# Kernel optimization log

Measured on AMD Instinct MI355X. Metric: run time of the kernel, lower is better.

## Reference

```python
import jax, jax.numpy as jnp
import numpy as np

B, S, H, NH = 2, 2048, 1024, 16
HD = H // NH
SCALE = float(H) ** 0.5  # note: source scales by sqrt(hidden_dim), not sqrt(head_dim)
EPS = 1e-5


def setup_inputs() -> dict:
    key = jax.random.key(0)
    ks = jax.random.split(key, 16)
    s = 0.02
    return {
        "q": jax.random.normal(ks[0], (B, S, H), jnp.float32),
        "k": jax.random.normal(ks[1], (B, S, H), jnp.float32),
        "v": jax.random.normal(ks[2], (B, S, H), jnp.float32),
        "mask": jax.random.randint(ks[3], (B, 1, S, S), 0, 2, jnp.int32),
        "Wq": jax.random.normal(ks[4], (H, H), jnp.float32) * s,
        "bq": jnp.zeros((H,), jnp.float32),
        "Wk": jax.random.normal(ks[5], (H, H), jnp.float32) * s,
        "bk": jnp.zeros((H,), jnp.float32),
        "Wv": jax.random.normal(ks[6], (H, H), jnp.float32) * s,
        "bv": jnp.zeros((H,), jnp.float32),
        "Wfc": jax.random.normal(ks[7], (H, H), jnp.float32) * s,
        "bfc": jnp.zeros((H,), jnp.float32),
        "gamma": jnp.ones((H,), jnp.float32),
        "beta": jnp.zeros((H,), jnp.float32),
    }


def reference(q, k, v, mask, Wq, bq, Wk, bk, Wv, bv, Wfc, bfc, gamma, beta):
    residual = q
    qh = (q @ Wq + bq).reshape(B, S, NH, HD)
    kh = (k @ Wk + bk).reshape(B, S, NH, HD)
    vh = (v @ Wv + bv).reshape(B, S, NH, HD)
    # full [B, NH, S, S] score matrix, as in the source
    energy = jnp.einsum('nqhd,nkhd->nhqk', qh, kh)
    energy = jnp.where(mask == 0, jnp.float32(-1e9), energy)
    attn = jax.nn.softmax(energy / SCALE, axis=3)  # dropout p=0.0 -> identity
    out = jnp.einsum('nhqk,nkhd->nqhd', attn, vh).reshape(B, S, H)
    y = out @ Wfc + bfc + residual
    mu = jnp.mean(y, axis=-1, keepdims=True)
    var = jnp.mean((y - mu) ** 2, axis=-1, keepdims=True)
    return gamma * (y - mu) / jnp.sqrt(var + EPS) + beta
```

## Files before the change

kernel.cpp:

```cpp
#include <hip/hip_runtime.h>
#include <hip/hip_bf16.h>

#define S_LEN  2048
#define HDIM   1024
#define NHEADS 16
#define HEADD  64
#define BATCH  2
#define MTOT   (BATCH * S_LEN)
#define K2EXP  0.04508422f

typedef __attribute__((ext_vector_type(8)))  __bf16 bf16x8;
typedef __attribute__((ext_vector_type(4)))  __bf16 bf16x4;
typedef __attribute__((ext_vector_type(4)))  float  f32x4;
typedef __attribute__((ext_vector_type(16))) float  f32x16;

__device__ __forceinline__ void gload16(const void* g, void* l) {
  __builtin_amdgcn_global_load_lds(
      (const __attribute__((address_space(1))) void*)g,
      (__attribute__((address_space(3))) void*)l, 16, 0, 0);
}
template<int STRIDE>
__device__ __forceinline__ bf16x8 lds_rdS(const __bf16* base, int row, int bcol) {
  const char* p = (const char*)base + row * STRIDE + (bcol ^ ((row & (STRIDE / 16 - 1)) << 4));
  return *(const bf16x8*)p;
}
__device__ __forceinline__ unsigned cvtpk_bf16(float lo, float hi) {
  unsigned r;
  asm("v_cvt_pk_bf16_f32 %0, %1, %2" : "=v"(r) : "v"(lo), "v"(hi));
  return r;
}
__device__ __forceinline__ void plswap(unsigned& a, unsigned& b) {
  asm volatile("v_permlane32_swap_b32 %0, %1" : "+v"(a), "+v"(b));
}

__global__ __launch_bounds__(256)
void prologue_kernel(const float* __restrict__ q, const float* __restrict__ k,
                     const float* __restrict__ v, const int* __restrict__ mask,
                     const float* __restrict__ Wq, const float* __restrict__ Wk,
                     const float* __restrict__ Wv, const float* __restrict__ Wfc,
                     __bf16* __restrict__ Qc, __bf16* __restrict__ Kc,
                     __bf16* __restrict__ Vc, unsigned* __restrict__ mbH,
                     __bf16* __restrict__ Wt)
{
  __shared__ float T[64][65];
  const int id = blockIdx.x;
  const int tid = threadIdx.x;
  if (id < 6144) {
    const int z = id >> 11, blk = id & 2047;
    const float* src = (z == 0) ? q : (z == 1) ? k : v;
    __bf16* dst = (z == 0) ? Qc : (z == 1) ? Kc : Vc;
    const size_t i = ((size_t)blk * 256 + tid) * 8;
    const float4 a = *(const float4*)&src[i];
    const float4 c = *(const float4*)&src[i + 4];
    bf16x8 o;
    o[0] = (__bf16)a.x; o[1] = (__bf16)a.y; o[2] = (__bf16)a.z; o[3] = (__bf16)a.w;
    o[4] = (__bf16)c.x; o[5] = (__bf16)c.y; o[6] = (__bf16)c.z; o[7] = (__bf16)c.w;
    *(bf16x8*)&dst[i] = o;
  } else if (id < 38912) {
    const size_t idx = (size_t)(id - 6144) * 256 + tid;
    const int m = mask[idx];
    const unsigned long long bal = __ballot(m != 0);
    const int lane = tid & 63;
    if ((lane & 31) == 0) {
      const int hh = lane >> 5;
      unsigned wlo = 0, whi = 0;
      #pragma unroll
      for (int j = 0; j < 16; ++j) {
        const int kvl = (j & 3) + 8 * (j >> 2) + 4 * hh;
        wlo |= (unsigned)((bal >> kvl) & 1ULL) << j;
        whi |= (unsigned)((bal >> (32 + kvl)) & 1ULL) << j;
      }
      const int b   = (int)(idx >> 22);
      const int qq  = (int)(idx >> 11) & 2047;
      const int seg = ((int)idx & 2047) >> 6;
      mbH[(((size_t)(hh * 2 + b)) * 32 + seg) * S_LEN + qq] = wlo | (whi << 16);
    }
  } else {
    const int f = id - 38912;
    const int z = f >> 8;
    const float* W = (z == 0) ? Wq : (z == 1) ? Wk : (z == 2) ? Wv : Wfc;
    const float sc = (z == 0) ? K2EXP : 1.0f;
    __bf16* O = Wt + (size_t)z * HDIM * HDIM;
    const int k0 = ((f >> 4) & 15) * 64, n0 = (f & 15) * 64;
    const int r  = tid >> 4;
    const int c4 = (tid & 15) * 4;
    #pragma unroll
    for (int p = 0; p < 4; ++p) {
      const int row = r + p * 16;
      const float4 vv = *(const float4*)&W[(size_t)(k0 + row) * HDIM + n0 + c4];
      T[row][c4 + 0] = vv.x; T[row][c4 + 1] = vv.y;
      T[row][c4 + 2] = vv.z; T[row][c4 + 3] = vv.w;
    }
    __syncthreads();
    #pragma unroll
    for (int p = 0; p < 4; ++p) {
      const int n = r + p * 16;
      bf16x4 o;
      #pragma unroll
      for (int i = 0; i < 4; ++i) o[i] = (__bf16)(T[c4 + i][n] * sc);
      *(bf16x4*)&O[(size_t)(n0 + n) * HDIM + k0 + c4] = o;
    }
  }
}

template<int MODE, int BMT>
__device__ __forceinline__ void gemm_body(
    __bf16* As, __bf16* Bs,
    const __bf16* __restrict__ A, const __bf16* __restrict__ Wt,
    const float* __restrict__ bias, float bscale,
    const float* __restrict__ resid,
    __bf16* __restrict__ Ob, float* __restrict__ Of, __bf16* __restrict__ Vtg)
{
  constexpr int AI = BMT / 32;
  const int tid = threadIdx.x, lane = tid & 63, w = tid >> 6;
  const int fr = lane & 15, k8 = (lane >> 4) * 8;
  const int wr = w >> 1, wc = w & 1;
  const int f   = blockIdx.x + gridDim.x * blockIdx.y;
  const int cpx = (gridDim.x * gridDim.y) >> 3;
  const int fs  = (f & 7) * cpx + (f >> 3);
  const int m0 = (fs / gridDim.x) * BMT, n0 = (fs % gridDim.x) * 128;
  const int srow8 = lane >> 3, slot = lane & 7;

  f32x4 acc[AI][4] = {};

  #define G_STAGE(kt, bf)                                                    \
    {                                                                        \
      _Pragma("unroll")                                                      \
      for (int c = 0; c < AI; ++c) {                                         \
        const int ra = w * (BMT / 4) + c * 8 + srow8;                        \
        gload16(&A[(size_t)(m0 + ra) * HDIM + (kt) * 64 + ((slot ^ (ra & 7)) * 8)], \
                (void*)&As[((bf) * BMT + ra) * 64]);                         \
      }                                                                      \
      _Pragma("unroll")                                                      \
      for (int c = 0; c < 4; ++c) {                                          \
        const int rb = w * 32 + c * 8 + srow8;                               \
        gload16(&Wt[(size_t)(n0 + rb) * HDIM + (kt) * 64 + ((slot ^ (rb & 7)) * 8)], \
                (void*)&Bs[((bf) * 128 + rb) * 64]);                         \
      }                                                                      \
    }

  #define G_COMPUTE(bf)                                                      \
    {                                                                        \
      _Pragma("unroll")                                                      \
      for (int kk = 0; kk < 64; kk += 32) {                                  \
        bf16x8 a[AI], b[4];                                                  \
        _Pragma("unroll")                                                    \
        for (int i = 0; i < AI; ++i)                                         \
          a[i] = lds_rdS<128>(&As[(bf) * BMT * 64], wr * (BMT / 2) + i * 16 + fr, (kk + k8) * 2); \
        _Pragma("unroll")                                                    \
        for (int j = 0; j < 4; ++j)                                          \
          b[j] = lds_rdS<128>(&Bs[(bf) * 128 * 64], wc * 64 + j * 16 + fr, (kk + k8) * 2); \
        _Pragma("unroll")                                                    \
        for (int i = 0; i < AI; ++i)                                         \
          _Pragma("unroll")                                                  \
          for (int j = 0; j < 4; ++j)                                        \
            acc[i][j] = __builtin_amdgcn_mfma_f32_16x16x32_bf16(a[i], b[j], acc[i][j], 0, 0, 0); \
      }                                                                      \
    }

  G_STAGE(0, 0)
  for (int kt = 0; kt < 15; ++kt) {
    G_STAGE(kt + 1, (kt + 1) & 1)
    if constexpr (BMT == 128) asm volatile("s_waitcnt vmcnt(8)" ::: "memory");
    else                      asm volatile("s_waitcnt vmcnt(6)" ::: "memory");
    __builtin_amdgcn_s_barrier();
    __builtin_amdgcn_sched_barrier(0);
    __builtin_amdgcn_s_setprio(1);
    G_COMPUTE(kt & 1)
    __builtin_amdgcn_s_setprio(0);
    __builtin_amdgcn_sched_barrier(0);
    __builtin_amdgcn_s_barrier();
  }
  asm volatile("s_waitcnt vmcnt(0)" ::: "memory");
  __builtin_amdgcn_s_barrier();
  G_COMPUTE(1)

  const int rg = (lane >> 4) * 4;
  #pragma unroll
  for (int i = 0; i < AI; ++i) {
    #pragma unroll
    for (int j = 0; j < 4; ++j) {
      const int col = n0 + wc * 64 + j * 16 + fr;
      if constexpr (MODE == 2) {
        const int h = col >> 6, hd = col & 63;
        const int row = m0 + wr * (BMT / 2) + i * 16 + rg;
        const int bq = row >> 11, qq = row & 2047;
        bf16x4 o;
        #pragma unroll
        for (int r = 0; r < 4; ++r) o[r] = (__bf16)(acc[i][j][r] + bias[col]);
        *(bf16x4*)&Vtg[(((size_t)bq * NHEADS + h) * HEADD + hd) * S_LEN + qq] = o;
      } else {
        #pragma unroll
        for (int r = 0; r < 4; ++r) {
          const int row = m0 + wr * (BMT / 2) + i * 16 + rg + r;
          if constexpr (MODE == 0) {
            Ob[(size_t)row * HDIM + col] = (__bf16)(acc[i][j][r] + bias[col] * bscale);
          } else {
            Of[(size_t)row * HDIM + col] =
                acc[i][j][r] + bias[col] + resid[(size_t)row * HDIM + col];
          }
        }
      }
    }
  }
  #undef G_STAGE
  #undef G_COMPUTE
}

__global__ __launch_bounds__(256)
void qkv_kernel(const __bf16* __restrict__ Qc, const __bf16* __restrict__ Kc,
                const __bf16* __restrict__ Vc, const __bf16* __restrict__ Wt,
                const float* __restrict__ bq, const float* __restrict__ bk,
                const float* __restrict__ bv,
                __bf16* __restrict__ Qb, __bf16* __restrict__ Kb,
                __bf16* __restrict__ Vtg)
{
  __shared__ __bf16 smem[2 * 128 * 64 * 2];
  __bf16* As = smem;
  __bf16* Bs = smem + 2 * 128 * 64;
  const int z = blockIdx.z;
  if (z == 2) {
    gemm_body<2, 128>(As, Bs, Vc, Wt + (size_t)2 * HDIM * HDIM, bv, 1.0f,
                      nullptr, nullptr, nullptr, Vtg);
  } else {
    gemm_body<0, 128>(As, Bs, z ? Kc : Qc, Wt + (size_t)z * HDIM * HDIM,
                      z ? bk : bq, z ? 1.0f : K2EXP, nullptr,
                      z ? Kb : Qb, nullptr, nullptr);
  }
}

__global__ __launch_bounds__(256)
void fc_kernel(const __bf16* __restrict__ A, const __bf16* __restrict__ Wt,
               const float* __restrict__ bias, const float* __restrict__ resid,
               float* __restrict__ Of)
{
  __shared__ __bf16 smem[2 * 64 * 64 + 2 * 128 * 64];
  __bf16* As = smem;
  __bf16* Bs = smem + 2 * 64 * 64;
  gemm_body<1, 64>(As, Bs, A, Wt + (size_t)3 * HDIM * HDIM, bias, 1.0f, resid,
                   nullptr, Of, nullptr);
}

__global__ __launch_bounds__(512)
void attn_kernel(const __bf16* __restrict__ Qb, const __bf16* __restrict__ Kb,
                 const __bf16* __restrict__ Vtg, const unsigned* __restrict__ mbH,
                 __bf16* __restrict__ AO)
{
  __shared__ __align__(16) char smem[49152];
  __bf16 (*Ks)[64][64] = (__bf16(*)[64][64])smem;
  __bf16 (*Vt)[64][64] = (__bf16(*)[64][64])(smem + 24576);

  const int bh = blockIdx.x, b = bh >> 4, h = bh & 15;
  const int tid = threadIdx.x, lane = tid & 63, w = tid >> 6;
  const int fr = lane & 31, hi = lane >> 5;
  const int qt = w >> 1, kvh = w & 1;
  const int qw = blockIdx.y * 128 + qt * 32;
  const int q  = qw + fr;

  bf16x8 qf[4];
  #pragma unroll
  for (int st = 0; st < 4; ++st)
    qf[st] = *(const bf16x8*)&Qb[((size_t)b * S_LEN + q) * HDIM + h * HEADD + st * 16 + hi * 8];

  const int srl = w * 8 + (lane >> 3);
  const int ssw = ((lane & 7) ^ (srl & 7)) * 8;
  const __bf16* ksrc = Kb  + ((size_t)b * S_LEN + srl) * HDIM + h * HEADD + ssw;
  const __bf16* vsrc = Vtg + ((size_t)bh * HEADD + srl) * S_LEN + ssw;
  const unsigned* tbl = mbH + ((size_t)(hi * 2 + b) * 32) * S_LEN + q;

  bf16x8 ones;
  #pragma unroll
  for (int e = 0; e < 8; ++e) ones[e] = (__bf16)1.0f;

  f32x16 o0 = {}, o1 = {}, l_acc = {};

  unsigned mv  = tbl[0];
  unsigned nmA = tbl[S_LEN];
  unsigned nmB = 0;
  gload16(ksrc,            (void*)&Ks[0][w * 8][0]);
  gload16(vsrc,            (void*)&Vt[0][w * 8][0]);
  gload16(ksrc + 64 * HDIM, (void*)&Ks[1][w * 8][0]);
  gload16(vsrc + 64,        (void*)&Vt[1][w * 8][0]);
  asm volatile("s_waitcnt vmcnt(2)" ::: "memory");
  __builtin_amdgcn_s_barrier();

  f32x16 s_cur = {};
  {
    const __bf16* Kb0 = &Ks[0][0][0];
    #pragma unroll
    for (int st = 0; st < 4; ++st)
      s_cur = __builtin_amdgcn_mfma_f32_32x32x16_bf16(
          lds_rdS<128>(Kb0, kvh * 32 + fr, st * 32 + hi * 16), qf[st], s_cur, 0, 0, 0);
  }

  int c0 = 0, c1 = 1, c2 = 2;
  for (int t = 0; t < 32; ++t) {
    asm volatile("s_waitcnt vmcnt(0)" ::: "memory");
    __builtin_amdgcn_s_barrier();
    __builtin_amdgcn_sched_barrier(0);

    if (t < 30) {
      gload16(ksrc + (size_t)(t + 2) * 64 * HDIM, (void*)&Ks[c2][w * 8][0]);
      gload16(vsrc + (size_t)(t + 2) * 64,        (void*)&Vt[c2][w * 8][0]);
      nmB = tbl[(size_t)(t + 2) * S_LEN];
    }

    f32x16 s_nxt = {};
    if (t < 31) {
      const __bf16* Kbn = &Ks[c1][0][0];
      __builtin_amdgcn_s_setprio(1);
      #pragma unroll
      for (int st = 0; st < 4; ++st)
        s_nxt = __builtin_amdgcn_mfma_f32_32x32x16_bf16(
            lds_rdS<128>(Kbn, kvh * 32 + fr, st * 32 + hi * 16), qf[st], s_nxt, 0, 0, 0);
      __builtin_amdgcn_s_setprio(0);
    }

    float pp[16];
    #pragma unroll
    for (int j = 0; j < 16; ++j) {
      const float e = __builtin_amdgcn_exp2f(s_cur[j]);
      const unsigned a = (unsigned)__builtin_amdgcn_sbfe(mv, j + 16 * kvh, 1);
      pp[j] = __uint_as_float(a & __float_as_uint(e));
    }
    bf16x8 pa[2];
    #pragma unroll
    for (int g = 0; g < 2; ++g) {
      const int o = g * 8;
      unsigned x  = cvtpk_bf16(pp[o + 0], pp[o + 1]);
      unsigned x2 = cvtpk_bf16(pp[o + 2], pp[o + 3]);
      unsigned y  = cvtpk_bf16(pp[o + 4], pp[o + 5]);
      unsigned y2 = cvtpk_bf16(pp[o + 6], pp[o + 7]);
      plswap(x, y);
      plswap(x2, y2);
      union { unsigned u[4]; bf16x8 v; } uu;
      uu.u[0] = x; uu.u[1] = x2; uu.u[2] = y; uu.u[3] = y2;
      pa[g] = uu.v;
    }

    {
      const __bf16* Vbc = &Vt[c0][0][0];
      __builtin_amdgcn_s_setprio(1);
      #pragma unroll
      for (int g = 0; g < 2; ++g) {
        const int bcol = kvh * 64 + g * 32 + hi * 16;
        l_acc = __builtin_amdgcn_mfma_f32_32x32x16_bf16(pa[g], ones, l_acc, 0, 0, 0);
        o0 = __builtin_amdgcn_mfma_f32_32x32x16_bf16(
            pa[g], lds_rdS<128>(Vbc, fr,      bcol), o0, 0, 0, 0);
        o1 = __builtin_amdgcn_mfma_f32_32x32x16_bf16(
            pa[g], lds_rdS<128>(Vbc, 32 + fr, bcol), o1, 0, 0, 0);
      }
      __builtin_amdgcn_s_setprio(0);
    }

    mv = nmA; nmA = nmB;
    s_cur = s_nxt;
    const int tmp = c0; c0 = c1; c1 = c2; c2 = tmp;
  }

  __builtin_amdgcn_s_barrier();
  float* sh = (float*)smem;
  const int li = qt * 64 + lane;
  if (kvh) {
    #pragma unroll
    for (int j = 0; j < 16; ++j) {
      sh[(j)      * 256 + li] = o0[j];
      sh[(16 + j) * 256 + li] = o1[j];
      sh[(32 + j) * 256 + li] = l_acc[j];
    }
  }
  __builtin_amdgcn_s_barrier();
  if (!kvh) {
    #pragma unroll
    for (int g = 0; g < 4; ++g) {
      #pragma unroll
      for (int r = 0; r < 4; ++r) {
        const int j = g * 4 + r;
        const float inv = __builtin_amdgcn_rcpf(l_acc[j] + sh[(32 + j) * 256 + li]);
        const int qq = qw + g * 8 + hi * 4 + r;
        AO[((size_t)b * S_LEN + qq) * HDIM + h * HEADD + fr]      =
            (__bf16)((o0[j] + sh[(j) * 256 + li]) * inv);
        AO[((size_t)b * S_LEN + qq) * HDIM + h * HEADD + 32 + fr] =
            (__bf16)((o1[j] + sh[(16 + j) * 256 + li]) * inv);
      }
    }
  }
}

__global__ __launch_bounds__(256)
void ln_kernel(float* __restrict__ y, const float* __restrict__ gamma,
               const float* __restrict__ beta)
{
  __shared__ float red[8];
  const int tid = threadIdx.x;
  float* p = y + (size_t)blockIdx.x * HDIM;

  float4 vv = *(const float4*)&p[tid * 4];
  float s  = vv.x + vv.y + vv.z + vv.w;
  float ss = vv.x * vv.x + vv.y * vv.y + vv.z * vv.z + vv.w * vv.w;
  #pragma unroll
  for (int d = 1; d < 64; d <<= 1) {
    s  += __shfl_xor(s, d);
    ss += __shfl_xor(ss, d);
  }
  const int wid = tid >> 6;
  if ((tid & 63) == 0) { red[wid * 2] = s; red[wid * 2 + 1] = ss; }
  __syncthreads();
  s  = red[0] + red[2] + red[4] + red[6];
  ss = red[1] + red[3] + red[5] + red[7];
  const float mean = s * (1.0f / HDIM);
  const float var  = ss * (1.0f / HDIM) - mean * mean;
  const float inv  = rsqrtf(var + 1e-5f);

  const float4 g  = *(const float4*)&gamma[tid * 4];
  const float4 bt = *(const float4*)&beta[tid * 4];
  vv.x = (vv.x - mean) * inv * g.x + bt.x;
  vv.y = (vv.y - mean) * inv * g.y + bt.y;
  vv.z = (vv.z - mean) * inv * g.z + bt.z;
  vv.w = (vv.w - mean) * inv * g.w + bt.w;
  *(float4*)&p[tid * 4] = vv;
}

extern "C" void kernel_launch(void* const* d_in, const int* in_sizes, int n_in,
                              void* d_out, int out_size, void* d_ws, size_t ws_size,
                              hipStream_t stream) {
  const float* q     = (const float*)d_in[0];
  const float* k     = (const float*)d_in[1];
  const float* v     = (const float*)d_in[2];
  const int*   mask  = (const int*)  d_in[3];
  const float* Wq    = (const float*)d_in[4];
  const float* bq    = (const float*)d_in[5];
  const float* Wk    = (const float*)d_in[6];
  const float* bk    = (const float*)d_in[7];
  const float* Wv    = (const float*)d_in[8];
  const float* bv    = (const float*)d_in[9];
  const float* Wfc   = (const float*)d_in[10];
  const float* bfc   = (const float*)d_in[11];
  const float* gamma = (const float*)d_in[12];
  const float* beta  = (const float*)d_in[13];
  float* out = (float*)d_out;

  char* ws = (char*)d_ws;
  const size_t MB16 = (size_t)MTOT * HDIM * 2;
  unsigned* mbH = (unsigned*)ws;
  __bf16* Wt  = (__bf16*)(ws + (1u << 20));
  __bf16* Qc  = (__bf16*)(ws + (1u << 20) + 4 * (size_t)HDIM * HDIM * 2);
  __bf16* Kc  = (__bf16*)((char*)Qc + MB16);
  __bf16* Vc  = (__bf16*)((char*)Kc + MB16);
  __bf16* Qb  = (__bf16*)((char*)Vc + MB16);
  __bf16* Kb  = (__bf16*)((char*)Qb + MB16);
  __bf16* Vtg = (__bf16*)((char*)Kb + MB16);
  __bf16* AO  = Kc;

  const dim3 blk(256);

  prologue_kernel<<<dim3(39936), blk, 0, stream>>>(
      q, k, v, mask, Wq, Wk, Wv, Wfc, Qc, Kc, Vc, mbH, Wt);

  qkv_kernel<<<dim3(HDIM / 128, MTOT / 128, 3), blk, 0, stream>>>(
      Qc, Kc, Vc, Wt, bq, bk, bv, Qb, Kb, Vtg);

  attn_kernel<<<dim3(BATCH * NHEADS, S_LEN / 128), dim3(512), 0, stream>>>(
      Qb, Kb, Vtg, mbH, AO);

  fc_kernel<<<dim3(HDIM / 128, MTOT / 64), blk, 0, stream>>>(
      AO, Wt, bfc, q, out);

  ln_kernel<<<dim3(MTOT), blk, 0, stream>>>(out, gamma, beta);
}
```

Before: 155.2 us.

## Fuse fp32-to-bf16 activation conversion into QKV GEMM A-tile loading

Removes the separate prologue pass that converted q/k/v from fp32 to bf16 in global memory. The QKV GEMM now loads fp32 A tiles into registers, converts them to bf16 and writes them into swizzled LDS, with a software-pipelined register prefetch. This avoids a full write and re-read of three bf16 activation copies, at the cost of more register pressure and A loads that go through VGPRs instead of direct global-to-LDS transfers. The FC kernel is inlined with the same logic, and AO now gets its own workspace slot.

```diff
diff --git a/kernel.cpp b/kernel.cpp
--- a/kernel.cpp
+++ b/kernel.cpp
@@ -34,30 +34,16 @@
 }
 
 __global__ __launch_bounds__(256)
-void prologue_kernel(const float* __restrict__ q, const float* __restrict__ k,
-                     const float* __restrict__ v, const int* __restrict__ mask,
+void prologue_kernel(const int* __restrict__ mask,
                      const float* __restrict__ Wq, const float* __restrict__ Wk,
                      const float* __restrict__ Wv, const float* __restrict__ Wfc,
-                     __bf16* __restrict__ Qc, __bf16* __restrict__ Kc,
-                     __bf16* __restrict__ Vc, unsigned* __restrict__ mbH,
-                     __bf16* __restrict__ Wt)
+                     unsigned* __restrict__ mbH, __bf16* __restrict__ Wt)
 {
   __shared__ float T[64][65];
   const int id = blockIdx.x;
   const int tid = threadIdx.x;
-  if (id < 6144) {
-    const int z = id >> 11, blk = id & 2047;
-    const float* src = (z == 0) ? q : (z == 1) ? k : v;
-    __bf16* dst = (z == 0) ? Qc : (z == 1) ? Kc : Vc;
-    const size_t i = ((size_t)blk * 256 + tid) * 8;
-    const float4 a = *(const float4*)&src[i];
-    const float4 c = *(const float4*)&src[i + 4];
-    bf16x8 o;
-    o[0] = (__bf16)a.x; o[1] = (__bf16)a.y; o[2] = (__bf16)a.z; o[3] = (__bf16)a.w;
-    o[4] = (__bf16)c.x; o[5] = (__bf16)c.y; o[6] = (__bf16)c.z; o[7] = (__bf16)c.w;
-    *(bf16x8*)&dst[i] = o;
-  } else if (id < 38912) {
-    const size_t idx = (size_t)(id - 6144) * 256 + tid;
+  if (id < 32768) {
+    const size_t idx = (size_t)id * 256 + tid;
     const int m = mask[idx];
     const unsigned long long bal = __ballot(m != 0);
     const int lane = tid & 63;
@@ -76,7 +62,7 @@
       mbH[(((size_t)(hh * 2 + b)) * 32 + seg) * S_LEN + qq] = wlo | (whi << 16);
     }
   } else {
-    const int f = id - 38912;
+    const int f = id - 32768;
     const int z = f >> 8;
     const float* W = (z == 0) ? Wq : (z == 1) ? Wk : (z == 2) ? Wv : Wfc;
     const float sc = (z == 0) ? K2EXP : 1.0f;
@@ -103,142 +89,205 @@
   }
 }
 
-template<int MODE, int BMT>
-__device__ __forceinline__ void gemm_body(
-    __bf16* As, __bf16* Bs,
-    const __bf16* __restrict__ A, const __bf16* __restrict__ Wt,
-    const float* __restrict__ bias, float bscale,
-    const float* __restrict__ resid,
-    __bf16* __restrict__ Ob, float* __restrict__ Of, __bf16* __restrict__ Vtg)
-{
-  constexpr int AI = BMT / 32;
-  const int tid = threadIdx.x, lane = tid & 63, w = tid >> 6;
-  const int fr = lane & 15, k8 = (lane >> 4) * 8;
-  const int wr = w >> 1, wc = w & 1;
-  const int f   = blockIdx.x + gridDim.x * blockIdx.y;
-  const int cpx = (gridDim.x * gridDim.y) >> 3;
-  const int fs  = (f & 7) * cpx + (f >> 3);
-  const int m0 = (fs / gridDim.x) * BMT, n0 = (fs % gridDim.x) * 128;
-  const int srow8 = lane >> 3, slot = lane & 7;
-
-  f32x4 acc[AI][4] = {};
-
-  #define G_STAGE(kt, bf)                                                    \
-    {                                                                        \
-      _Pragma("unroll")                                                      \
-      for (int c = 0; c < AI; ++c) {                                         \
-        const int ra = w * (BMT / 4) + c * 8 + srow8;                        \
-        gload16(&A[(size_t)(m0 + ra) * HDIM + (kt) * 64 + ((slot ^ (ra & 7)) * 8)], \
-                (void*)&As[((bf) * BMT + ra) * 64]);                         \
-      }                                                                      \
-      _Pragma("unroll")                                                      \
-      for (int c = 0; c < 4; ++c) {                                          \
-        const int rb = w * 32 + c * 8 + srow8;                               \
-        gload16(&Wt[(size_t)(n0 + rb) * HDIM + (kt) * 64 + ((slot ^ (rb & 7)) * 8)], \
-                (void*)&Bs[((bf) * 128 + rb) * 64]);                         \
-      }                                                                      \
-    }
-
-  #define G_COMPUTE(bf)                                                      \
-    {                                                                        \
-      _Pragma("unroll")                                                      \
-      for (int kk = 0; kk < 64; kk += 32) {                                  \
-        bf16x8 a[AI], b[4];                                                  \
-        _Pragma("unroll")                                                    \
-        for (int i = 0; i < AI; ++i)                                         \
-          a[i] = lds_rdS<128>(&As[(bf) * BMT * 64], wr * (BMT / 2) + i * 16 + fr, (kk + k8) * 2); \
-        _Pragma("unroll")                                                    \
-        for (int j = 0; j < 4; ++j)                                          \
-          b[j] = lds_rdS<128>(&Bs[(bf) * 128 * 64], wc * 64 + j * 16 + fr, (kk + k8) * 2); \
-        _Pragma("unroll")                                                    \
-        for (int i = 0; i < AI; ++i)                                         \
-          _Pragma("unroll")                                                  \
-          for (int j = 0; j < 4; ++j)                                        \
-            acc[i][j] = __builtin_amdgcn_mfma_f32_16x16x32_bf16(a[i], b[j], acc[i][j], 0, 0, 0); \
-      }                                                                      \
-    }
-
-  G_STAGE(0, 0)
-  for (int kt = 0; kt < 15; ++kt) {
-    G_STAGE(kt + 1, (kt + 1) & 1)
-    if constexpr (BMT == 128) asm volatile("s_waitcnt vmcnt(8)" ::: "memory");
-    else                      asm volatile("s_waitcnt vmcnt(6)" ::: "memory");
-    __builtin_amdgcn_s_barrier();
-    __builtin_amdgcn_sched_barrier(0);
-    __builtin_amdgcn_s_setprio(1);
-    G_COMPUTE(kt & 1)
-    __builtin_amdgcn_s_setprio(0);
-    __builtin_amdgcn_sched_barrier(0);
-    __builtin_amdgcn_s_barrier();
-  }
-  asm volatile("s_waitcnt vmcnt(0)" ::: "memory");
-  __builtin_amdgcn_s_barrier();
-  G_COMPUTE(1)
-
-  const int rg = (lane >> 4) * 4;
-  #pragma unroll
-  for (int i = 0; i < AI; ++i) {
-    #pragma unroll
-    for (int j = 0; j < 4; ++j) {
-      const int col = n0 + wc * 64 + j * 16 + fr;
-      if constexpr (MODE == 2) {
-        const int h = col >> 6, hd = col & 63;
-        const int row = m0 + wr * (BMT / 2) + i * 16 + rg;
-        const int bq = row >> 11, qq = row & 2047;
-        bf16x4 o;
-        #pragma unroll
-        for (int r = 0; r < 4; ++r) o[r] = (__bf16)(acc[i][j][r] + bias[col]);
-        *(bf16x4*)&Vtg[(((size_t)bq * NHEADS + h) * HEADD + hd) * S_LEN + qq] = o;
-      } else {
-        #pragma unroll
-        for (int r = 0; r < 4; ++r) {
-          const int row = m0 + wr * (BMT / 2) + i * 16 + rg + r;
-          if constexpr (MODE == 0) {
-            Ob[(size_t)row * HDIM + col] = (__bf16)(acc[i][j][r] + bias[col] * bscale);
-          } else {
-            Of[(size_t)row * HDIM + col] =
-                acc[i][j][r] + bias[col] + resid[(size_t)row * HDIM + col];
-          }
-        }
-      }
-    }
-  }
-  #undef G_STAGE
-  #undef G_COMPUTE
-}
-
 __global__ __launch_bounds__(256)
-void qkv_kernel(const __bf16* __restrict__ Qc, const __bf16* __restrict__ Kc,
-                const __bf16* __restrict__ Vc, const __bf16* __restrict__ Wt,
+void qkv_kernel(const float* __restrict__ q, const float* __restrict__ k,
+                const float* __restrict__ v, const __bf16* __restrict__ Wt,
                 const float* __restrict__ bq, const float* __restrict__ bk,
                 const float* __restrict__ bv,
                 __bf16* __restrict__ Qb, __bf16* __restrict__ Kb,
                 __bf16* __restrict__ Vtg)
 {
-  __shared__ __bf16 smem[2 * 128 * 64 * 2];
-  __bf16* As = smem;
-  __bf16* Bs = smem + 2 * 128 * 64;
+  __shared__ __bf16 As[2][128][64];
+  __shared__ __bf16 Bs[2][128][64];
   const int z = blockIdx.z;
-  if (z == 2) {
-    gemm_body<2, 128>(As, Bs, Vc, Wt + (size_t)2 * HDIM * HDIM, bv, 1.0f,
-                      nullptr, nullptr, nullptr, Vtg);
-  } else {
-    gemm_body<0, 128>(As, Bs, z ? Kc : Qc, Wt + (size_t)z * HDIM * HDIM,
-                      z ? bk : bq, z ? 1.0f : K2EXP, nullptr,
-                      z ? Kb : Qb, nullptr, nullptr);
-  }
+  const float* A    = (z == 0) ? q  : (z == 1) ? k  : v;
+  const float* bias = (z == 0) ? bq : (z == 1) ? bk : bv;
+  const float bscale = (z == 0) ? K2EXP : 1.0f;
+  const __bf16* Wz = Wt + (size_t)z * HDIM * HDIM;
+
+  const int tid = threadIdx.x, lane = tid & 63, w = tid >> 6;
+  const int fr = lane & 15, k8 = (lane >> 4) * 8;
+  const int wr = w >> 1, wc = w & 1;
+  const int f   = blockIdx.x + 8 * blockIdx.y;
+  const int fs  = (f & 7) * 32 + (f >> 3);
+  const int m0 = (fs >> 3) * 128, n0 = (fs & 7) * 128;
+  const int srow8 = lane >> 3, slot = lane & 7;
+  const int ar = tid >> 1, ahf = tid & 1;
+  const float* asrc = A + (size_t)(m0 + ar) * HDIM + ahf * 32;
+
+  f32x4 acc[4][4] = {};
+  float4 areg[8];
+
+  #define Q_LOADA(kt)                                                        \
+    { _Pragma("unroll")                                                      \
+      for (int i = 0; i < 8; ++i)                                            \
+        areg[i] = *(const float4*)(asrc + (kt) * 64 + i * 4); }
+  #define Q_STB(kt, bf)                                                      \
+    { _Pragma("unroll")                                                      \
+      for (int c = 0; c < 4; ++c) {                                          \
+        const int rb = w * 32 + c * 8 + srow8;                               \
+        gload16(&Wz[(size_t)(n0 + rb) * HDIM + (kt) * 64 + ((slot ^ (rb & 7)) * 8)], \
+                (void*)&Bs[bf][rb][0]);                                      \
+      } }
+  #define Q_WRA(bf)                                                          \
+    { _Pragma("unroll")                                                      \
+      for (int s = 0; s < 4; ++s) {                                          \
+        bf16x8 o;                                                            \
+        o[0] = (__bf16)areg[2*s].x;   o[1] = (__bf16)areg[2*s].y;            \
+        o[2] = (__bf16)areg[2*s].z;   o[3] = (__bf16)areg[2*s].w;            \
+        o[4] = (__bf16)areg[2*s+1].x; o[5] = (__bf16)areg[2*s+1].y;          \
+        o[6] = (__bf16)areg[2*s+1].z; o[7] = (__bf16)areg[2*s+1].w;          \
+        *(bf16x8*)((char*)&As[bf][ar][0] +                                   \
+                   ((ahf * 64 + s * 16) ^ ((ar & 7) << 4))) = o;             \
+      } }
+  #define Q_COMPUTE(bf)                                                      \
+    { _Pragma("unroll")                                                      \
+      for (int kk = 0; kk < 64; kk += 32) {                                  \
+        bf16x8 a[4], b[4];                                                   \
+        _Pragma("unroll")                                                    \
+        for (int i = 0; i < 4; ++i)                                          \
+          a[i] = lds_rdS<128>(&As[bf][0][0], wr * 64 + i * 16 + fr, (kk + k8) * 2); \
+        _Pragma("unroll")                                                    \
+        for (int j = 0; j < 4; ++j)                                          \
+          b[j] = lds_rdS<128>(&Bs[bf][0][0], wc * 64 + j * 16 + fr, (kk + k8) * 2); \
+        _Pragma("unroll")                                                    \
+        for (int i = 0; i < 4; ++i)                                          \
+          _Pragma("unroll")                                                  \
+          for (int j = 0; j < 4; ++j)                                        \
+            acc[i][j] = __builtin_amdgcn_mfma_f32_16x16x32_bf16(a[i], b[j], acc[i][j], 0, 0, 0); \
+      } }
+
+  Q_LOADA(0)
+  Q_STB(0, 0)
+  asm volatile("s_waitcnt vmcnt(4)" ::: "memory");
+  Q_WRA(0)
+  asm volatile("s_waitcnt vmcnt(0) lgkmcnt(0)" ::: "memory");
+  __builtin_amdgcn_s_barrier();
+
+  for (int kt = 0; kt < 15; ++kt) {
+    const int buf = kt & 1;
+    Q_LOADA(kt + 1)
+    Q_STB(kt + 1, buf ^ 1)
+    __builtin_amdgcn_s_setprio(1);
+    Q_COMPUTE(buf)
+    __builtin_amdgcn_s_setprio(0);
+    asm volatile("s_waitcnt vmcnt(4)" ::: "memory");
+    Q_WRA(buf ^ 1)
+    asm volatile("s_waitcnt vmcnt(0) lgkmcnt(0)" ::: "memory");
+    __builtin_amdgcn_s_barrier();
+  }
+  Q_COMPUTE(1)
+
+  const int rg = (lane >> 4) * 4;
+  #pragma unroll
+  for (int i = 0; i < 4; ++i) {
+    #pragma unroll
+    for (int j = 0; j < 4; ++j) {
+      const int col = n0 + wc * 64 + j * 16 + fr;
+      if (z == 2) {
+        const int h = col >> 6, hd = col & 63;
+        const int row = m0 + wr * 64 + i * 16 + rg;
+        const int bq2 = row >> 11, qq = row & 2047;
+        bf16x4 o;
+        #pragma unroll
+        for (int r = 0; r < 4; ++r) o[r] = (__bf16)(acc[i][j][r] + bias[col]);
+        *(bf16x4*)&Vtg[(((size_t)bq2 * NHEADS + h) * HEADD + hd) * S_LEN + qq] = o;
+      } else {
+        __bf16* O = (z == 0) ? Qb : Kb;
+        #pragma unroll
+        for (int r = 0; r < 4; ++r) {
+          const int row = m0 + wr * 64 + i * 16 + rg + r;
+          O[(size_t)row * HDIM + col] = (__bf16)(acc[i][j][r] + bias[col] * bscale);
+        }
+      }
+    }
+  }
+  #undef Q_LOADA
+  #undef Q_STB
+  #undef Q_WRA
+  #undef Q_COMPUTE
 }
 
 __global__ __launch_bounds__(256)
-void fc_kernel(const __bf16* __restrict__ A, const __bf16* __restrict__ Wt,
+void fc_kernel(const __bf16* __restrict__ Ab, const __bf16* __restrict__ Wt,
                const float* __restrict__ bias, const float* __restrict__ resid,
                float* __restrict__ Of)
 {
-  __shared__ __bf16 smem[2 * 64 * 64 + 2 * 128 * 64];
-  __bf16* As = smem;
-  __bf16* Bs = smem + 2 * 64 * 64;
-  gemm_body<1, 64>(As, Bs, A, Wt + (size_t)3 * HDIM * HDIM, bias, 1.0f, resid,
-                   nullptr, Of, nullptr);
+  __shared__ __bf16 As[2][64][64];
+  __shared__ __bf16 Bs[2][128][64];
+  const __bf16* Wz = Wt + (size_t)3 * HDIM * HDIM;
+  const int tid = threadIdx.x, lane = tid & 63, w = tid >> 6;
+  const int fr = lane & 15, k8 = (lane >> 4) * 8;
+  const int wr = w >> 1, wc = w & 1;
+  const int f   = blockIdx.x + 8 * blockIdx.y;
+  const int fs  = (f & 7) * 64 + (f >> 3);
+  const int m0 = (fs >> 3) * 64, n0 = (fs & 7) * 128;
+  const int srow8 = lane >> 3, slot = lane & 7;
+
+  f32x4 acc[2][4] = {};
+
+  #define F_STAGE(kt, bf)                                                    \
+    { _Pragma("unroll")                                                      \
+      for (int c = 0; c < 2; ++c) {                                          \
+        const int ra = w * 16 + c * 8 + srow8;                               \
+        gload16(&Ab[(size_t)(m0 + ra) * HDIM + (kt) * 64 + ((slot ^ (ra & 7)) * 8)], \
+                (void*)&As[bf][ra][0]);                                      \
+      }                                                                      \
+      _Pragma("unroll")                                                      \
+      for (int c = 0; c < 4; ++c) {                                          \
+        const int rb = w * 32 + c * 8 + srow8;                               \
+        gload16(&Wz[(size_t)(n0 + rb) * HDIM + (kt) * 64 + ((slot ^ (rb & 7)) * 8)], \
+                (void*)&Bs[bf][rb][0]);                                      \
+      } }
+  #define F_COMPUTE(bf)                                                      \
+    { _Pragma("unroll")                                                      \
+      for (int kk = 0; kk < 64; kk += 32) {                                  \
+        bf16x8 a[2], b[4];                                                   \
+        _Pragma("unroll")                                                    \
+        for (int i = 0; i < 2; ++i)                                          \
+          a[i] = lds_rdS<128>(&As[bf][0][0], wr * 32 + i * 16 + fr, (kk + k8) * 2); \
+        _Pragma("unroll")                                                    \
+        for (int j = 0; j < 4; ++j)                                          \
+          b[j] = lds_rdS<128>(&Bs[bf][0][0], wc * 64 + j * 16 + fr, (kk + k8) * 2); \
+        _Pragma("unroll")                                                    \
+        for (int i = 0; i < 2; ++i)                                          \
+          _Pragma("unroll")                                                  \
+          for (int j = 0; j < 4; ++j)                                        \
+            acc[i][j] = __builtin_amdgcn_mfma_f32_16x16x32_bf16(a[i], b[j], acc[i][j], 0, 0, 0); \
+      } }
+
+  F_STAGE(0, 0)
+  for (int kt = 0; kt < 15; ++kt) {
+    F_STAGE(kt + 1, (kt + 1) & 1)
+    asm volatile("s_waitcnt vmcnt(6)" ::: "memory");
+    __builtin_amdgcn_s_barrier();
+    __builtin_amdgcn_sched_barrier(0);
+    __builtin_amdgcn_s_setprio(1);
+    F_COMPUTE(kt & 1)
+    __builtin_amdgcn_s_setprio(0);
+    __builtin_amdgcn_sched_barrier(0);
+    __builtin_amdgcn_s_barrier();
+  }
+  asm volatile("s_waitcnt vmcnt(0)" ::: "memory");
+  __builtin_amdgcn_s_barrier();
+  F_COMPUTE(1)
+
+  const int rg = (lane >> 4) * 4;
+  #pragma unroll
+  for (int i = 0; i < 2; ++i) {
+    #pragma unroll
+    for (int j = 0; j < 4; ++j) {
+      const int col = n0 + wc * 64 + j * 16 + fr;
+      #pragma unroll
+      for (int r = 0; r < 4; ++r) {
+        const int row = m0 + wr * 32 + i * 16 + rg + r;
+        Of[(size_t)row * HDIM + col] =
+            acc[i][j][r] + bias[col] + resid[(size_t)row * HDIM + col];
+      }
+    }
+  }
+  #undef F_STAGE
+  #undef F_COMPUTE
 }
 
 __global__ __launch_bounds__(512)
@@ -277,8 +326,8 @@
   unsigned mv  = tbl[0];
   unsigned nmA = tbl[S_LEN];
   unsigned nmB = 0;
-  gload16(ksrc,            (void*)&Ks[0][w * 8][0]);
-  gload16(vsrc,            (void*)&Vt[0][w * 8][0]);
+  gload16(ksrc,             (void*)&Ks[0][w * 8][0]);
+  gload16(vsrc,             (void*)&Vt[0][w * 8][0]);
   gload16(ksrc + 64 * HDIM, (void*)&Ks[1][w * 8][0]);
   gload16(vsrc + 64,        (void*)&Vt[1][w * 8][0]);
   asm volatile("s_waitcnt vmcnt(2)" ::: "memory");
@@ -444,26 +493,23 @@
   const size_t MB16 = (size_t)MTOT * HDIM * 2;
   unsigned* mbH = (unsigned*)ws;
   __bf16* Wt  = (__bf16*)(ws + (1u << 20));
-  __bf16* Qc  = (__bf16*)(ws + (1u << 20) + 4 * (size_t)HDIM * HDIM * 2);
-  __bf16* Kc  = (__bf16*)((char*)Qc + MB16);
-  __bf16* Vc  = (__bf16*)((char*)Kc + MB16);
-  __bf16* Qb  = (__bf16*)((char*)Vc + MB16);
+  __bf16* Qb  = (__bf16*)(ws + (1u << 20) + 4 * (size_t)HDIM * HDIM * 2);
   __bf16* Kb  = (__bf16*)((char*)Qb + MB16);
   __bf16* Vtg = (__bf16*)((char*)Kb + MB16);
-  __bf16* AO  = Kc;
+  __bf16* AO  = (__bf16*)((char*)Vtg + MB16);
 
   const dim3 blk(256);
 
-  prologue_kernel<<<dim3(39936), blk, 0, stream>>>(
-      q, k, v, mask, Wq, Wk, Wv, Wfc, Qc, Kc, Vc, mbH, Wt);
-
-  qkv_kernel<<<dim3(HDIM / 128, MTOT / 128, 3), blk, 0, stream>>>(
-      Qc, Kc, Vc, Wt, bq, bk, bv, Qb, Kb, Vtg);
+  prologue_kernel<<<dim3(33792), blk, 0, stream>>>(
+      mask, Wq, Wk, Wv, Wfc, mbH, Wt);
+
+  qkv_kernel<<<dim3(8, 32, 3), blk, 0, stream>>>(
+      q, k, v, Wt, bq, bk, bv, Qb, Kb, Vtg);
 
   attn_kernel<<<dim3(BATCH * NHEADS, S_LEN / 128), dim3(512), 0, stream>>>(
       Qb, Kb, Vtg, mbH, AO);
 
-  fc_kernel<<<dim3(HDIM / 128, MTOT / 64), blk, 0, stream>>>(
+  fc_kernel<<<dim3(8, 64), blk, 0, stream>>>(
       AO, Wt, bfc, q, out);
 
   ln_kernel<<<dim3(MTOT), blk, 0, stream>>>(out, gamma, beta);
```

After: 186.7 us. 1.2x slower.
